# Kernel optimization log

Hardware: AMD Instinct MI355X
Metric: run time of the kernel (lower is better)

## Reference

```python
import jax, jax.numpy as jnp
import numpy as np

EMBED = 256      # hp.embed_size
ATT = 256        # hp.attention_size
KSZ = 5          # hp.kernel_size
L = 4            # hp.decoder_layers
N_MELS = 80
R = 4
KEY_PR = (4096 // 4) / 512.0   # hp.max_frames // hp.r / hp.max_timesteps = 2.0
QUERY_PR = 1.0
SQRT_HALF = float(np.sqrt(0.5))


def _pos_enc(T, C, pos_rate):
    # Faithful to source: angle_rates = pos*pos_rate/10000^(2*(k//2)/C); pe = pos*angle_rates
    pos = jnp.arange(T, dtype=jnp.float32)[:, None]            # [T,1]
    k = jnp.arange(C)[None, :]                                  # [1,C]
    power = jnp.power(jnp.float32(10000.0), 2.0 * (k // 2).astype(jnp.float32) / C)
    angle = pos * (pos * pos_rate / power)                      # [T,C]
    return jnp.where(k % 2 == 0, jnp.sin(angle), jnp.cos(angle))[None]  # [1,T,C]


def _conv_block(x, w, b, dilation):
    # causal dilated Conv1D + GLU + scaled residual. x:[B,T,C], w:[K,C,2C]
    pad = (KSZ - 1) * dilation
    y = jax.lax.conv_general_dilated(
        x, w, window_strides=(1,), padding=[(pad, 0)], rhs_dilation=(dilation,),
        dimension_numbers=('NWC', 'WIO', 'NWC')) + b
    a, g = jnp.split(y, 2, axis=-1)
    return (x + a * jax.nn.sigmoid(g)) * SQRT_HALF


def _attention(x, keys, values, w1, b1, w2, b2, w3, b3, wo, bo):
    Tq, Tk, C = x.shape[1], keys.shape[1], x.shape[-1]
    q = x + _pos_enc(Tq, C, QUERY_PR)
    k = keys + _pos_enc(Tk, C, KEY_PR)
    k_out = k @ w1 + b1           # fc1(keys)
    q_out = q @ w2 + b2           # fc2(query)
    v_out = values @ w3 + b3      # fc3(values)
    aw = jnp.einsum('bqd,bkd->bqk', q_out, k_out)
    # key_masks = ones_like(sum(keys_out,-1)) -> never zero, masking is a no-op (kept faithful)
    al = jax.nn.softmax(aw, axis=-1)  # dropout disabled (training=False)
    ctx = jnp.einsum('bqk,bkd->bqd', al, v_out) * jax.lax.rsqrt(jnp.float32(Tk))
    return ctx @ wo + bo


def setup_inputs() -> dict:
    key = jax.random.key(0)
    ks = jax.random.split(key, 16)
    s = jnp.float32(0.02)
    B, TQ, TK = 32, 1024, 512
    d = {}
    d['inputs'] = jax.random.normal(ks[0], (B, TQ, N_MELS * R), jnp.float32)
    d['keys'] = jax.random.normal(ks[1], (B, TK, EMBED), jnp.float32)
    d['values'] = jax.random.normal(ks[2], (B, TK, EMBED), jnp.float32)
    d['w_first'] = jax.random.normal(ks[3], (N_MELS * R, EMBED), jnp.float32) * s
    d['b_first'] = jnp.zeros((EMBED,), jnp.float32)
    d['fc_w'] = jax.random.normal(ks[4], (L - 1, EMBED, EMBED), jnp.float32) * s
    d['fc_b'] = jnp.zeros((L - 1, EMBED), jnp.float32)
    d['conv_w'] = jax.random.normal(ks[5], (L, KSZ, EMBED, 2 * EMBED), jnp.float32) * s
    d['conv_b'] = jnp.zeros((L, 2 * EMBED), jnp.float32)
    d['att_w1'] = jax.random.normal(ks[6], (L, EMBED, ATT), jnp.float32) * s
    d['att_b1'] = jnp.zeros((L, ATT), jnp.float32)
    d['att_w2'] = jax.random.normal(ks[7], (L, EMBED, ATT), jnp.float32) * s
    d['att_b2'] = jnp.zeros((L, ATT), jnp.float32)
    d['att_w3'] = jax.random.normal(ks[8], (L, EMBED, ATT), jnp.float32) * s
    d['att_b3'] = jnp.zeros((L, ATT), jnp.float32)
    d['att_wo'] = jax.random.normal(ks[9], (L, ATT, EMBED), jnp.float32) * s
    d['att_bo'] = jnp.zeros((L, EMBED), jnp.float32)
    d['w_done'] = jax.random.normal(ks[10], (EMBED, 2), jnp.float32) * s
    d['b_done'] = jnp.zeros((2,), jnp.float32)
    d['w_mel'] = jax.random.normal(ks[11], (EMBED, N_MELS * R), jnp.float32) * s
    d['b_mel'] = jnp.zeros((N_MELS * R,), jnp.float32)
    return d


def reference(inputs, keys, values, w_first, b_first, fc_w, fc_b, conv_w, conv_b,
              att_w1, att_b1, att_w2, att_b2, att_w3, att_b3, att_wo, att_bo,
              w_done, b_done, w_mel, b_mel):
    h = jax.nn.relu(inputs @ w_first + b_first)
    for i in range(L - 1):
        h = jax.nn.relu(h @ fc_w[i] + fc_b[i])
    for i in range(L):
        h = _conv_block(h, conv_w[i], conv_b[i], 2 ** i)
        att = _attention(h, keys, values,
                         att_w1[i], att_b1[i], att_w2[i], att_b2[i],
                         att_w3[i], att_b3[i], att_wo[i], att_bo[i])
        h = (att + h) * SQRT_HALF
    done_output = jax.nn.sigmoid(h @ w_done + b_done)
    mel_output = h @ w_mel + b_mel
    return (mel_output, done_output, h)
```

## Files before the change

### kernel.cpp

```cpp
#include <hip/hip_runtime.h>
#include <hip/hip_bf16.h>
#include <math.h>

#define SQH 0.70710678118654752440f

typedef __bf16 bf16x8 __attribute__((ext_vector_type(8)));
typedef float f32x4 __attribute__((ext_vector_type(4)));

__device__ __forceinline__ void glds16(const void* g, void* l) {
    __builtin_amdgcn_global_load_lds((const __attribute__((address_space(1))) void*)g,
                                     (__attribute__((address_space(3))) void*)l, 16, 0, 0);
}
__device__ __forceinline__ void wait_vm0_barrier() {
    asm volatile("s_waitcnt vmcnt(0)" ::: "memory");
    __builtin_amdgcn_s_barrier();
}

__device__ __forceinline__ int xcd_swz(int lin, int n) {
    if (n & 7) return lin;
    return (lin & 7) * (n >> 3) + (lin >> 3);
}

__global__ void pos_enc_kernel(float* __restrict__ pe, int T, float rate) {
    int idx = blockIdx.x * blockDim.x + threadIdx.x;
    if (idx >= T * 256) return;
    int t = idx >> 8;
    int k = idx & 255;
    float e = 2.0f * (float)(k >> 1) / 256.0f;
    float pw = powf(10000.0f, e);
    float ang = (float)t * ((float)t * rate / pw);
    pe[idx] = ((k & 1) == 0) ? sinf(ang) : cosf(ang);
}

__global__ void zero_init(float* z) { z[threadIdx.x] = 0.f; }

__global__ __launch_bounds__(256) void cvt_bf(const float* __restrict__ src,
                                              __bf16* __restrict__ dst, long n8) {
    long i = (long)blockIdx.x * 256 + threadIdx.x;
    if (i >= n8) return;
    const float* s = src + i * 8;
    float4 a = *(const float4*)s, b = *(const float4*)(s + 4);
    bf16x8 o;
    o[0] = (__bf16)a.x; o[1] = (__bf16)a.y; o[2] = (__bf16)a.z; o[3] = (__bf16)a.w;
    o[4] = (__bf16)b.x; o[5] = (__bf16)b.y; o[6] = (__bf16)b.z; o[7] = (__bf16)b.w;
    *(bf16x8*)(dst + i * 8) = o;
}

__global__ __launch_bounds__(256) void kpe_kernel(const float* __restrict__ keys,
                                                  const float* __restrict__ pek,
                                                  __bf16* __restrict__ dst) {
    long i = (long)blockIdx.x * 256 + threadIdx.x;
    long row = i >> 5; int c8 = (int)(i & 31) << 3;
    const float* kp = keys + row * 256 + c8;
    const float* pp = pek + (row & 511) * 256 + c8;
    float4 a = *(const float4*)kp, b = *(const float4*)(kp + 4);
    float4 p = *(const float4*)pp, q = *(const float4*)(pp + 4);
    bf16x8 o;
    o[0] = (__bf16)(a.x + p.x); o[1] = (__bf16)(a.y + p.y);
    o[2] = (__bf16)(a.z + p.z); o[3] = (__bf16)(a.w + p.w);
    o[4] = (__bf16)(b.x + q.x); o[5] = (__bf16)(b.y + q.y);
    o[6] = (__bf16)(b.z + q.z); o[7] = (__bf16)(b.w + q.w);
    *(bf16x8*)(dst + i * 8) = o;
}

__global__ __launch_bounds__(256) void transpose_k(const float* __restrict__ src,
                                                   __bf16* __restrict__ dst,
                                                   int R, int Cc, long sS, long sD) {
    __shared__ float tile[32][33];
    src += (long)blockIdx.z * sS;
    dst += (long)blockIdx.z * sD;
    int c0 = blockIdx.x * 32, r0 = blockIdx.y * 32;
    int tx = threadIdx.x & 31, ty = threadIdx.x >> 5;
#pragma unroll
    for (int p = 0; p < 4; ++p)
        tile[ty + 8 * p][tx] = src[(long)(r0 + ty + 8 * p) * Cc + c0 + tx];
    __syncthreads();
#pragma unroll
    for (int p = 0; p < 4; ++p)
        dst[(long)(c0 + ty + 8 * p) * R + r0 + tx] = (__bf16)tile[tx][ty + 8 * p];
}

template<int BIAS_MODE, int ACT, int OUT_MODE, int RES>
__global__ __launch_bounds__(256) void gemm_bf(
    const __bf16* __restrict__ A, const __bf16* __restrict__ Bt,
    const float* __restrict__ bias, const float* __restrict__ res,
    float* __restrict__ outF, __bf16* __restrict__ outB,
    int M, int N, int K, long sA, long sB, long sC)
{
    __shared__ __align__(16) __bf16 As[2][4096];
    __shared__ __align__(16) __bf16 Bs[2][4096];
    const int gx = gridDim.x, gy = gridDim.y;
    int lin = (blockIdx.z * gy + blockIdx.y) * gx + blockIdx.x;
    lin = xcd_swz(lin, gx * gy * gridDim.z);
    const int bx = lin % gx, by = (lin / gx) % gy, z = lin / (gx * gy);
    A += (long)z * sA;
    Bt += (long)z * sB;
    const int row0 = by << 7, col0 = bx << 7;
    const int tid = threadIdx.x, wid = tid >> 6, lane = tid & 63;
    const int lrow = lane & 15, lkp = lane >> 4;
    const int wm = (wid >> 1) << 6, wn = (wid & 1) << 6;
    const int srow = (wid << 5) + (lane >> 2);
    const int kq8 = (lane & 3) << 3;
    const __bf16* Ap0 = A + (long)(row0 + srow) * K + kq8;
    const __bf16* Ap1 = Ap0 + (long)16 * K;
    int c0i = col0 + srow, c1i = col0 + srow + 16;
    if (c0i > N - 1) c0i = N - 1;
    if (c1i > N - 1) c1i = N - 1;
    const __bf16* Bp0 = Bt + (long)c0i * K + kq8;
    const __bf16* Bp1 = Bt + (long)c1i * K + kq8;

    auto stage = [&](int b, int k0) {
        __bf16* A_ = As[b] + (wid << 10);
        __bf16* B_ = Bs[b] + (wid << 10);
        glds16(Ap0 + k0, A_);
        glds16(Ap1 + k0, A_ + 512);
        glds16(Bp0 + k0, B_);
        glds16(Bp1 + k0, B_ + 512);
    };

    f32x4 acc[4][4];
#pragma unroll
    for (int i = 0; i < 4; ++i)
#pragma unroll
        for (int j = 0; j < 4; ++j) acc[i][j] = (f32x4){0.f, 0.f, 0.f, 0.f};

    const int nk = K >> 5;
    stage(0, 0);
    wait_vm0_barrier();
    int cur = 0;
    for (int t = 0; t < nk; ++t) {
        if (t + 1 < nk) stage(cur ^ 1, (t + 1) << 5);
        bf16x8 af[4], bfr[4];
        const __bf16* Ar = As[cur] + (wm + lrow) * 32 + lkp * 8;
        const __bf16* Br = Bs[cur] + (wn + lrow) * 32 + lkp * 8;
#pragma unroll
        for (int i = 0; i < 4; ++i) af[i] = *(const bf16x8*)(Ar + i * 512);
#pragma unroll
        for (int j = 0; j < 4; ++j) bfr[j] = *(const bf16x8*)(Br + j * 512);
#pragma unroll
        for (int i = 0; i < 4; ++i)
#pragma unroll
            for (int j = 0; j < 4; ++j)
                acc[i][j] = __builtin_amdgcn_mfma_f32_16x16x32_bf16(af[i], bfr[j], acc[i][j], 0, 0, 0);
        wait_vm0_barrier();
        cur ^= 1;
    }

    float* oF = outF ? outF + (long)z * sC : nullptr;
    __bf16* oB = outB ? outB + (long)z * sC : nullptr;
    const float* resp = RES ? res + (long)z * sC : nullptr;
#pragma unroll
    for (int i = 0; i < 4; ++i) {
#pragma unroll
        for (int r = 0; r < 4; ++r) {
            const int gr = row0 + wm + i * 16 + lkp * 4 + r;
#pragma unroll
            for (int j = 0; j < 4; ++j) {
                const int gc = col0 + wn + j * 16 + lrow;
                if (gc >= N) continue;
                float v = acc[i][j][r];
                if (BIAS_MODE == 1) v += bias[gc];
                if (BIAS_MODE == 2) v += bias[gr];
                if (RES) v = (v + resp[(long)gr * N + gc]) * SQH;
                if (ACT == 1) v = fmaxf(v, 0.f);
                if (OUT_MODE == 0 || OUT_MODE == 2) oF[(long)gr * N + gc] = v;
                if (OUT_MODE == 1 || OUT_MODE == 2) oB[(long)gr * N + gc] = (__bf16)v;
            }
        }
    }
}

__global__ __launch_bounds__(256) void conv_glu(
    const __bf16* __restrict__ hbf, const float* __restrict__ hin,
    const __bf16* __restrict__ Wt, const float* __restrict__ bias,
    const float* __restrict__ peq,
    float* __restrict__ hc_f, __bf16* __restrict__ hc_b, __bf16* __restrict__ hq_b,
    int dil, const __bf16* __restrict__ zp)
{
    __shared__ __align__(16) __bf16 As[2][4096];
    __shared__ __align__(16) __bf16 Bas[2][2048];
    __shared__ __align__(16) __bf16 Bgs[2][2048];
    const int gx = gridDim.x;
    int lin = blockIdx.y * gx + blockIdx.x;
    lin = xcd_swz(lin, gx * gridDim.y);
    const int bx = lin % gx, by = lin / gx;
    const int row0 = by << 7, col0 = bx << 6;
    const int tid = threadIdx.x, wid = tid >> 6, lane = tid & 63;
    const int lrow = lane & 15, lkp = lane >> 4;
    const int wr = wid >> 1, wc = wid & 1;
    const int sA = (wid << 5) + (lane >> 2);
    const int kq8 = (lane & 3) << 3;
    const int grow = row0 + sA;
    const int t0 = (row0 & 1023) + sA;
    const int cB = col0 + (wid << 4) + (lane >> 2);
    const __bf16* Ba0 = Wt + (long)cB * 1280 + kq8;
    const __bf16* Bg0 = Wt + (long)(cB + 256) * 1280 + kq8;

    auto stage = [&](int b, int k0) {
        const int tap = k0 >> 8;
        const int off = (4 - tap) * dil;
        const int kc = (k0 & 255) + kq8;
        const __bf16* a0 = (t0 >= off) ? hbf + (long)(grow - off) * 256 + kc : zp;
        const __bf16* a1 = (t0 + 16 >= off) ? hbf + (long)(grow + 16 - off) * 256 + kc : zp;
        __bf16* A_ = As[b] + (wid << 10);
        glds16(a0, A_);
        glds16(a1, A_ + 512);
        glds16(Ba0 + k0, Bas[b] + (wid << 9));
        glds16(Bg0 + k0, Bgs[b] + (wid << 9));
    };

    f32x4 aca[4][2], acg[4][2];
#pragma unroll
    for (int i = 0; i < 4; ++i)
#pragma unroll
        for (int j = 0; j < 2; ++j) {
            aca[i][j] = (f32x4){0.f, 0.f, 0.f, 0.f};
            acg[i][j] = (f32x4){0.f, 0.f, 0.f, 0.f};
        }

    stage(0, 0);
    wait_vm0_barrier();
    int cur = 0;
    for (int t = 0; t < 40; ++t) {
        if (t + 1 < 40) stage(cur ^ 1, (t + 1) << 5);
        bf16x8 af[4], ba[2], bg[2];
        const __bf16* Ar = As[cur] + ((wr << 6) + lrow) * 32 + lkp * 8;
        const __bf16* Bar = Bas[cur] + ((wc << 5) + lrow) * 32 + lkp * 8;
        const __bf16* Bgr = Bgs[cur] + ((wc << 5) + lrow) * 32 + lkp * 8;
#pragma unroll
        for (int i = 0; i < 4; ++i) af[i] = *(const bf16x8*)(Ar + i * 512);
#pragma unroll
        for (int j = 0; j < 2; ++j) { ba[j] = *(const bf16x8*)(Bar + j * 512); bg[j] = *(const bf16x8*)(Bgr + j * 512); }
#pragma unroll
        for (int i = 0; i < 4; ++i)
#pragma unroll
            for (int j = 0; j < 2; ++j) {
                aca[i][j] = __builtin_amdgcn_mfma_f32_16x16x32_bf16(af[i], ba[j], aca[i][j], 0, 0, 0);
                acg[i][j] = __builtin_amdgcn_mfma_f32_16x16x32_bf16(af[i], bg[j], acg[i][j], 0, 0, 0);
            }
        wait_vm0_barrier();
        cur ^= 1;
    }
#pragma unroll
    for (int i = 0; i < 4; ++i) {
#pragma unroll
        for (int r = 0; r < 4; ++r) {
            const int gr = row0 + (wr << 6) + i * 16 + lkp * 4 + r;
            const long rb = (long)gr * 256;
            const long pb = (long)(gr & 1023) * 256;
#pragma unroll
            for (int j = 0; j < 2; ++j) {
                const int ca = col0 + (wc << 5) + j * 16 + lrow;
                float a = aca[i][j][r] + bias[ca];
                float g = acg[i][j][r] + bias[ca + 256];
                float v = (hin[rb + ca] + a / (1.f + expf(-g))) * SQH;
                hc_f[rb + ca] = v;
                hc_b[rb + ca] = (__bf16)v;
                hq_b[rb + ca] = (__bf16)(v + peq[pb + ca]);
            }
        }
    }
}

__global__ __launch_bounds__(512) void scores_sm(
    const __bf16* __restrict__ Q, const __bf16* __restrict__ Kb,
    __bf16* __restrict__ aw)
{
    __shared__ __align__(16) __bf16 As[2][128 * 32];
    __shared__ __align__(16) __bf16 Bs[2][512 * 32];
    __shared__ float redM[4][128];
    __shared__ float redS[4][128];
    int lin = xcd_swz(blockIdx.x, gridDim.x);
    const int rt = lin & 7, z = lin >> 3;
    const int row0 = rt << 7;
    const __bf16* Az = Q + (long)z * 1024 * 256;
    const __bf16* Bz = Kb + (long)z * 512 * 256;
    __bf16* awz = aw + (long)z * 1024 * 512;
    const int tid = threadIdx.x, wid = tid >> 6, lane = tid & 63;
    const int lrow = lane & 15, lkp = lane >> 4;
    const int wr = wid >> 2, wc = wid & 3;
    const int sr = lane >> 2;
    const int kq8 = (lane & 3) << 3;

    auto stage = [&](int b, int k0) {
        glds16(Az + (long)(row0 + (wid << 4) + sr) * 256 + k0 + kq8, As[b] + (wid << 9));
#pragma unroll
        for (int c = 0; c < 4; ++c) {
            const int R = ((c << 3) + wid) << 4;
            glds16(Bz + (long)(R + sr) * 256 + k0 + kq8, Bs[b] + (R << 5));
        }
    };

    f32x4 acc[4][8];
#pragma unroll
    for (int i = 0; i < 4; ++i)
#pragma unroll
        for (int j = 0; j < 8; ++j) acc[i][j] = (f32x4){0.f, 0.f, 0.f, 0.f};

    stage(0, 0);
    wait_vm0_barrier();
    int cur = 0;
    for (int t = 0; t < 8; ++t) {
        if (t + 1 < 8) stage(cur ^ 1, (t + 1) << 5);
        bf16x8 af[4], bfr[8];
        const __bf16* Ar = As[cur] + ((wr << 6) + lrow) * 32 + lkp * 8;
        const __bf16* Br = Bs[cur] + ((wc << 7) + lrow) * 32 + lkp * 8;
#pragma unroll
        for (int i = 0; i < 4; ++i) af[i] = *(const bf16x8*)(Ar + i * 512);
#pragma unroll
        for (int j = 0; j < 8; ++j) bfr[j] = *(const bf16x8*)(Br + j * 512);
#pragma unroll
        for (int i = 0; i < 4; ++i)
#pragma unroll
            for (int j = 0; j < 8; ++j)
                acc[i][j] = __builtin_amdgcn_mfma_f32_16x16x32_bf16(af[i], bfr[j], acc[i][j], 0, 0, 0);
        wait_vm0_barrier();
        cur ^= 1;
    }

    float mx[4][4];
#pragma unroll
    for (int i = 0; i < 4; ++i)
#pragma unroll
        for (int r = 0; r < 4; ++r) {
            float m = acc[i][0][r];
#pragma unroll
            for (int j = 1; j < 8; ++j) m = fmaxf(m, acc[i][j][r]);
#pragma unroll
            for (int s = 1; s < 16; s <<= 1) m = fmaxf(m, __shfl_xor(m, s));
            mx[i][r] = m;
        }
    if (lrow == 0) {
#pragma unroll
        for (int i = 0; i < 4; ++i)
#pragma unroll
            for (int r = 0; r < 4; ++r)
                redM[wc][(wr << 6) + i * 16 + (lkp << 2) + r] = mx[i][r];
    }
    __syncthreads();
    float sm[4][4];
#pragma unroll
    for (int i = 0; i < 4; ++i)
#pragma unroll
        for (int r = 0; r < 4; ++r) {
            const int row = (wr << 6) + i * 16 + (lkp << 2) + r;
            float m = fmaxf(fmaxf(redM[0][row], redM[1][row]), fmaxf(redM[2][row], redM[3][row]));
            float s = 0.f;
#pragma unroll
            for (int j = 0; j < 8; ++j) {
                float p = expf(acc[i][j][r] - m);
                acc[i][j][r] = p;
                s += p;
            }
#pragma unroll
            for (int sft = 1; sft < 16; sft <<= 1) s += __shfl_xor(s, sft);
            sm[i][r] = s;
        }
    if (lrow == 0) {
#pragma unroll
        for (int i = 0; i < 4; ++i)
#pragma unroll
            for (int r = 0; r < 4; ++r)
                redS[wc][(wr << 6) + i * 16 + (lkp << 2) + r] = sm[i][r];
    }
    __syncthreads();
#pragma unroll
    for (int i = 0; i < 4; ++i)
#pragma unroll
        for (int r = 0; r < 4; ++r) {
            const int row = (wr << 6) + i * 16 + (lkp << 2) + r;
            float S = redS[0][row] + redS[1][row] + redS[2][row] + redS[3][row];
            float sc = 0.04419417382415922f / S;
            __bf16* op = awz + (long)(row0 + row) * 512 + (wc << 7) + lrow;
#pragma unroll
            for (int j = 0; j < 8; ++j)
                op[j * 16] = (__bf16)(acc[i][j][r] * sc);
        }
}

__global__ __launch_bounds__(256) void done_kernel(const float* __restrict__ h,
                                                   const float* __restrict__ w,
                                                   const float* __restrict__ b,
                                                   float* __restrict__ out) {
    int row = blockIdx.x * 4 + (threadIdx.x >> 6);
    int lane = threadIdx.x & 63;
    float4 hv = *(const float4*)(h + (long)row * 256 + lane * 4);
    float4 w0 = *(const float4*)(w + lane * 8);
    float4 w1 = *(const float4*)(w + lane * 8 + 4);
    float d0 = hv.x * w0.x + hv.y * w0.z + hv.z * w1.x + hv.w * w1.z;
    float d1 = hv.x * w0.y + hv.y * w0.w + hv.z * w1.y + hv.w * w1.w;
#pragma unroll
    for (int s = 32; s; s >>= 1) { d0 += __shfl_xor(d0, s); d1 += __shfl_xor(d1, s); }
    if (lane == 0) {
        out[(long)row * 2 + 0] = 1.f / (1.f + expf(-(d0 + b[0])));
        out[(long)row * 2 + 1] = 1.f / (1.f + expf(-(d1 + b[1])));
    }
}

extern "C" void kernel_launch(void* const* d_in, const int* in_sizes, int n_in,
                              void* d_out, int out_size, void* d_ws, size_t ws_size,
                              hipStream_t stream) {
    const float* inputs  = (const float*)d_in[0];
    const float* keys    = (const float*)d_in[1];
    const float* values  = (const float*)d_in[2];
    const float* w_first = (const float*)d_in[3];
    const float* b_first = (const float*)d_in[4];
    const float* fc_w    = (const float*)d_in[5];
    const float* fc_b    = (const float*)d_in[6];
    const float* conv_w  = (const float*)d_in[7];
    const float* conv_b  = (const float*)d_in[8];
    const float* w1 = (const float*)d_in[9];  const float* b1 = (const float*)d_in[10];
    const float* w2 = (const float*)d_in[11]; const float* b2 = (const float*)d_in[12];
    const float* w3 = (const float*)d_in[13]; const float* b3 = (const float*)d_in[14];
    const float* wo = (const float*)d_in[15]; const float* bo = (const float*)d_in[16];
    const float* w_done = (const float*)d_in[17]; const float* b_done = (const float*)d_in[18];
    const float* w_mel  = (const float*)d_in[19]; const float* b_mel  = (const float*)d_in[20];
    float* out = (float*)d_out;
    float* ws  = (float*)d_ws;

    float* peq  = ws;
    float* pek  = peq + 262144;
    float* zp   = pek + 131072;
    float* h_f  = zp + 64;
    float* hc_f = h_f + 8388608;
    __bf16* h_b   = (__bf16*)(hc_f + 8388608);
    __bf16* hc_b  = h_b   + 8388608;
    __bf16* hq_b  = hc_b  + 8388608;
    __bf16* q_bf  = hq_b  + 8388608;
    __bf16* k_bf  = q_bf  + 8388608;
    __bf16* kpe_bf= k_bf  + 4194304;
    __bf16* val_bf= kpe_bf+ 4194304;
    __bf16* vT_bf = val_bf+ 4194304;
    __bf16* awb   = vT_bf + 4194304;
    __bf16* wfT   = awb   + 16777216;
    __bf16* fcT   = wfT   + 81920;
    __bf16* convT = fcT   + 196608;
    __bf16* w1T   = convT + 2621440;
    __bf16* w2T   = w1T   + 262144;
    __bf16* w3T   = w2T   + 262144;
    __bf16* woT   = w3T   + 262144;
    __bf16* wmT   = woT   + 262144;
    __bf16* in_bf = awb;
    __bf16* ctx_bf = q_bf;

    dim3 blk(256);

    pos_enc_kernel<<<1024, 256, 0, stream>>>(peq, 1024, 1.0f);
    pos_enc_kernel<<<512, 256, 0, stream>>>(pek, 512, 2.0f);
    zero_init<<<1, 64, 0, stream>>>(zp);

    cvt_bf<<<5120, 256, 0, stream>>>(inputs, in_bf, 1310720);
    cvt_bf<<<2048, 256, 0, stream>>>(values, val_bf, 524288);
    kpe_kernel<<<2048, 256, 0, stream>>>(keys, pek, kpe_bf);

    transpose_k<<<dim3(8, 10, 1), blk, 0, stream>>>(w_first, wfT, 320, 256, 0, 0);
    transpose_k<<<dim3(8, 8, 3), blk, 0, stream>>>(fc_w, fcT, 256, 256, 65536, 65536);
    transpose_k<<<dim3(16, 40, 4), blk, 0, stream>>>(conv_w, convT, 1280, 512, 655360, 655360);
    transpose_k<<<dim3(8, 8, 4), blk, 0, stream>>>(w1, w1T, 256, 256, 65536, 65536);
    transpose_k<<<dim3(8, 8, 4), blk, 0, stream>>>(w2, w2T, 256, 256, 65536, 65536);
    transpose_k<<<dim3(8, 8, 4), blk, 0, stream>>>(w3, w3T, 256, 256, 65536, 65536);
    transpose_k<<<dim3(8, 8, 4), blk, 0, stream>>>(wo, woT, 256, 256, 65536, 65536);
    transpose_k<<<dim3(10, 8, 1), blk, 0, stream>>>(w_mel, wmT, 256, 320, 0, 0);

    gemm_bf<1, 1, 1, 0><<<dim3(2, 256, 1), blk, 0, stream>>>(
        in_bf, wfT, b_first, nullptr, nullptr, h_b, 32768, 256, 320, 0, 0, 0);
    gemm_bf<1, 1, 1, 0><<<dim3(2, 256, 1), blk, 0, stream>>>(
        h_b, fcT + 0 * 65536, fc_b + 0 * 256, nullptr, nullptr, hq_b, 32768, 256, 256, 0, 0, 0);
    gemm_bf<1, 1, 1, 0><<<dim3(2, 256, 1), blk, 0, stream>>>(
        hq_b, fcT + 1 * 65536, fc_b + 1 * 256, nullptr, nullptr, hc_b, 32768, 256, 256, 0, 0, 0);
    gemm_bf<1, 1, 2, 0><<<dim3(2, 256, 1), blk, 0, stream>>>(
        hc_b, fcT + 2 * 65536, fc_b + 2 * 256, nullptr, h_f, h_b, 32768, 256, 256, 0, 0, 0);

    for (int l = 0; l < 4; ++l) {
        int dil = 1 << l;
        conv_glu<<<dim3(4, 256, 1), blk, 0, stream>>>(
            h_b, h_f, convT + (long)l * 655360, conv_b + l * 512, peq,
            hc_f, hc_b, hq_b, dil, (const __bf16*)zp);
        gemm_bf<1, 0, 1, 0><<<dim3(2, 256, 1), blk, 0, stream>>>(
            hq_b, w2T + (long)l * 65536, b2 + l * 256, nullptr, nullptr, q_bf, 32768, 256, 256, 0, 0, 0);
        gemm_bf<1, 0, 1, 0><<<dim3(2, 128, 1), blk, 0, stream>>>(
            kpe_bf, w1T + (long)l * 65536, b1 + l * 256, nullptr, nullptr, k_bf, 16384, 256, 256, 0, 0, 0);
        gemm_bf<2, 0, 1, 0><<<dim3(4, 2, 32), blk, 0, stream>>>(
            w3T + (long)l * 65536, val_bf, b3 + l * 256, nullptr, nullptr, vT_bf,
            256, 512, 256, 0, 512 * 256, 256 * 512);
        scores_sm<<<256, 512, 0, stream>>>(q_bf, k_bf, awb);
        gemm_bf<0, 0, 1, 0><<<dim3(2, 8, 32), blk, 0, stream>>>(
            awb, vT_bf, nullptr, nullptr, nullptr, ctx_bf,
            1024, 256, 512, 1024 * 512, 256 * 512, 1024 * 256);
        gemm_bf<1, 0, 2, 1><<<dim3(2, 256, 1), blk, 0, stream>>>(
            ctx_bf, woT + (long)l * 65536, bo + l * 256, hc_f, h_f, h_b, 32768, 256, 256, 0, 0, 0);
    }

    gemm_bf<1, 0, 0, 0><<<dim3(3, 256, 1), blk, 0, stream>>>(
        h_b, wmT, b_mel, nullptr, out, nullptr, 32768, 320, 256, 0, 0, 0);
    done_kernel<<<8192, 256, 0, stream>>>(h_f, w_done, b_done, out + 10485760);
    hipMemcpyAsync(out + 10551296, h_f, (size_t)8388608 * 4, hipMemcpyDeviceToDevice, stream);
}
```

Before: 1.236 ms.

## Overlap prefetch with compute, reorder LDS staging, batch key projections

The GEMM, conv_glu and scores kernels now wait only for the current stage's loads (vmcnt(4)/vmcnt(5)) before the barrier. The next stage's global-to-LDS loads can then overlap the MFMA work instead of being drained at the end of each iteration. Lane-to-row mapping for staging and the LDS read addressing change to a k-major layout, which may reduce bank conflicts. All four layers' key projections (fc1 of keys) are computed in one batched launch up front, and the unused hc_b bf16 store is dropped. The partial vmcnt wait depends on how many loads are in flight and on in-order completion, which risks correctness if the counts are wrong.

```diff
diff --git a/kernel.cpp b/kernel.cpp
--- a/kernel.cpp
+++ b/kernel.cpp
@@ -10,10 +10,6 @@
 __device__ __forceinline__ void glds16(const void* g, void* l) {
     __builtin_amdgcn_global_load_lds((const __attribute__((address_space(1))) void*)g,
                                      (__attribute__((address_space(3))) void*)l, 16, 0, 0);
-}
-__device__ __forceinline__ void wait_vm0_barrier() {
-    asm volatile("s_waitcnt vmcnt(0)" ::: "memory");
-    __builtin_amdgcn_s_barrier();
 }
 
 __device__ __forceinline__ int xcd_swz(int lin, int n) {
@@ -85,7 +81,7 @@
     const __bf16* __restrict__ A, const __bf16* __restrict__ Bt,
     const float* __restrict__ bias, const float* __restrict__ res,
     float* __restrict__ outF, __bf16* __restrict__ outB,
-    int M, int N, int K, long sA, long sB, long sC)
+    int M, int N, int K, long sA, long sB, long sC, long sBias, int zmB)
 {
     __shared__ __align__(16) __bf16 As[2][4096];
     __shared__ __align__(16) __bf16 Bs[2][4096];
@@ -94,13 +90,14 @@
     lin = xcd_swz(lin, gx * gy * gridDim.z);
     const int bx = lin % gx, by = (lin / gx) % gy, z = lin / (gx * gy);
     A += (long)z * sA;
-    Bt += (long)z * sB;
+    Bt += (long)(z % zmB) * sB;
+    bias = bias ? bias + (long)z * sBias : bias;
     const int row0 = by << 7, col0 = bx << 7;
     const int tid = threadIdx.x, wid = tid >> 6, lane = tid & 63;
     const int lrow = lane & 15, lkp = lane >> 4;
     const int wm = (wid >> 1) << 6, wn = (wid & 1) << 6;
-    const int srow = (wid << 5) + (lane >> 2);
-    const int kq8 = (lane & 3) << 3;
+    const int srow = (wid << 5) + (lane & 15);
+    const int kq8 = (lane >> 4) << 3;
     const __bf16* Ap0 = A + (long)(row0 + srow) * K + kq8;
     const __bf16* Ap1 = Ap0 + (long)16 * K;
     int c0i = col0 + srow, c1i = col0 + srow + 16;
@@ -125,24 +122,30 @@
         for (int j = 0; j < 4; ++j) acc[i][j] = (f32x4){0.f, 0.f, 0.f, 0.f};
 
     const int nk = K >> 5;
+    const int ab = (wm >> 4), bb = (wn >> 4);
     stage(0, 0);
-    wait_vm0_barrier();
     int cur = 0;
     for (int t = 0; t < nk; ++t) {
-        if (t + 1 < nk) stage(cur ^ 1, (t + 1) << 5);
+        if (t + 1 < nk) {
+            stage(cur ^ 1, (t + 1) << 5);
+            asm volatile("s_waitcnt vmcnt(4)" ::: "memory");
+        } else {
+            asm volatile("s_waitcnt vmcnt(0)" ::: "memory");
+        }
+        __builtin_amdgcn_s_barrier();
         bf16x8 af[4], bfr[4];
-        const __bf16* Ar = As[cur] + (wm + lrow) * 32 + lkp * 8;
-        const __bf16* Br = Bs[cur] + (wn + lrow) * 32 + lkp * 8;
-#pragma unroll
-        for (int i = 0; i < 4; ++i) af[i] = *(const bf16x8*)(Ar + i * 512);
-#pragma unroll
-        for (int j = 0; j < 4; ++j) bfr[j] = *(const bf16x8*)(Br + j * 512);
+#pragma unroll
+        for (int i = 0; i < 4; ++i)
+            af[i] = *(const bf16x8*)(As[cur] + (ab + i) * 512 + lkp * 128 + lrow * 8);
+#pragma unroll
+        for (int j = 0; j < 4; ++j)
+            bfr[j] = *(const bf16x8*)(Bs[cur] + (bb + j) * 512 + lkp * 128 + lrow * 8);
 #pragma unroll
         for (int i = 0; i < 4; ++i)
 #pragma unroll
             for (int j = 0; j < 4; ++j)
                 acc[i][j] = __builtin_amdgcn_mfma_f32_16x16x32_bf16(af[i], bfr[j], acc[i][j], 0, 0, 0);
-        wait_vm0_barrier();
+        __builtin_amdgcn_s_barrier();
         cur ^= 1;
     }
 
@@ -174,7 +177,7 @@
     const __bf16* __restrict__ hbf, const float* __restrict__ hin,
     const __bf16* __restrict__ Wt, const float* __restrict__ bias,
     const float* __restrict__ peq,
-    float* __restrict__ hc_f, __bf16* __restrict__ hc_b, __bf16* __restrict__ hq_b,
+    float* __restrict__ hc_f, __bf16* __restrict__ hq_b,
     int dil, const __bf16* __restrict__ zp)
 {
     __shared__ __align__(16) __bf16 As[2][4096];
@@ -188,11 +191,11 @@
     const int tid = threadIdx.x, wid = tid >> 6, lane = tid & 63;
     const int lrow = lane & 15, lkp = lane >> 4;
     const int wr = wid >> 1, wc = wid & 1;
-    const int sA = (wid << 5) + (lane >> 2);
-    const int kq8 = (lane & 3) << 3;
-    const int grow = row0 + sA;
-    const int t0 = (row0 & 1023) + sA;
-    const int cB = col0 + (wid << 4) + (lane >> 2);
+    const int srowA = (wid << 5) + (lane & 15);
+    const int kq8 = (lane >> 4) << 3;
+    const int grow = row0 + srowA;
+    const int t0 = (row0 & 1023) + srowA;
+    const int cB = col0 + (wid << 4) + (lane & 15);
     const __bf16* Ba0 = Wt + (long)cB * 1280 + kq8;
     const __bf16* Bg0 = Wt + (long)(cB + 256) * 1280 + kq8;
 
@@ -219,18 +222,24 @@
         }
 
     stage(0, 0);
-    wait_vm0_barrier();
     int cur = 0;
     for (int t = 0; t < 40; ++t) {
-        if (t + 1 < 40) stage(cur ^ 1, (t + 1) << 5);
+        if (t + 1 < 40) {
+            stage(cur ^ 1, (t + 1) << 5);
+            asm volatile("s_waitcnt vmcnt(4)" ::: "memory");
+        } else {
+            asm volatile("s_waitcnt vmcnt(0)" ::: "memory");
+        }
+        __builtin_amdgcn_s_barrier();
         bf16x8 af[4], ba[2], bg[2];
-        const __bf16* Ar = As[cur] + ((wr << 6) + lrow) * 32 + lkp * 8;
-        const __bf16* Bar = Bas[cur] + ((wc << 5) + lrow) * 32 + lkp * 8;
-        const __bf16* Bgr = Bgs[cur] + ((wc << 5) + lrow) * 32 + lkp * 8;
-#pragma unroll
-        for (int i = 0; i < 4; ++i) af[i] = *(const bf16x8*)(Ar + i * 512);
-#pragma unroll
-        for (int j = 0; j < 2; ++j) { ba[j] = *(const bf16x8*)(Bar + j * 512); bg[j] = *(const bf16x8*)(Bgr + j * 512); }
+#pragma unroll
+        for (int i = 0; i < 4; ++i)
+            af[i] = *(const bf16x8*)(As[cur] + ((wr << 2) + i) * 512 + lkp * 128 + lrow * 8);
+#pragma unroll
+        for (int j = 0; j < 2; ++j) {
+            ba[j] = *(const bf16x8*)(Bas[cur] + ((wc << 1) + j) * 512 + lkp * 128 + lrow * 8);
+            bg[j] = *(const bf16x8*)(Bgs[cur] + ((wc << 1) + j) * 512 + lkp * 128 + lrow * 8);
+        }
 #pragma unroll
         for (int i = 0; i < 4; ++i)
 #pragma unroll
@@ -238,7 +247,7 @@
                 aca[i][j] = __builtin_amdgcn_mfma_f32_16x16x32_bf16(af[i], ba[j], aca[i][j], 0, 0, 0);
                 acg[i][j] = __builtin_amdgcn_mfma_f32_16x16x32_bf16(af[i], bg[j], acg[i][j], 0, 0, 0);
             }
-        wait_vm0_barrier();
+        __builtin_amdgcn_s_barrier();
         cur ^= 1;
     }
 #pragma unroll
@@ -255,7 +264,6 @@
                 float g = acg[i][j][r] + bias[ca + 256];
                 float v = (hin[rb + ca] + a / (1.f + expf(-g))) * SQH;
                 hc_f[rb + ca] = v;
-                hc_b[rb + ca] = (__bf16)v;
                 hq_b[rb + ca] = (__bf16)(v + peq[pb + ca]);
             }
         }
@@ -279,8 +287,8 @@
     const int tid = threadIdx.x, wid = tid >> 6, lane = tid & 63;
     const int lrow = lane & 15, lkp = lane >> 4;
     const int wr = wid >> 2, wc = wid & 3;
-    const int sr = lane >> 2;
-    const int kq8 = (lane & 3) << 3;
+    const int sr = lane & 15;
+    const int kq8 = (lane >> 4) << 3;
 
     auto stage = [&](int b, int k0) {
         glds16(Az + (long)(row0 + (wid << 4) + sr) * 256 + k0 + kq8, As[b] + (wid << 9));
@@ -298,23 +306,28 @@
         for (int j = 0; j < 8; ++j) acc[i][j] = (f32x4){0.f, 0.f, 0.f, 0.f};
 
     stage(0, 0);
-    wait_vm0_barrier();
     int cur = 0;
     for (int t = 0; t < 8; ++t) {
-        if (t + 1 < 8) stage(cur ^ 1, (t + 1) << 5);
+        if (t + 1 < 8) {
+            stage(cur ^ 1, (t + 1) << 5);
+            asm volatile("s_waitcnt vmcnt(5)" ::: "memory");
+        } else {
+            asm volatile("s_waitcnt vmcnt(0)" ::: "memory");
+        }
+        __builtin_amdgcn_s_barrier();
         bf16x8 af[4], bfr[8];
-        const __bf16* Ar = As[cur] + ((wr << 6) + lrow) * 32 + lkp * 8;
-        const __bf16* Br = Bs[cur] + ((wc << 7) + lrow) * 32 + lkp * 8;
-#pragma unroll
-        for (int i = 0; i < 4; ++i) af[i] = *(const bf16x8*)(Ar + i * 512);
-#pragma unroll
-        for (int j = 0; j < 8; ++j) bfr[j] = *(const bf16x8*)(Br + j * 512);
+#pragma unroll
+        for (int i = 0; i < 4; ++i)
+            af[i] = *(const bf16x8*)(As[cur] + ((wr << 2) + i) * 512 + lkp * 128 + lrow * 8);
+#pragma unroll
+        for (int j = 0; j < 8; ++j)
+            bfr[j] = *(const bf16x8*)(Bs[cur] + ((wc << 3) + j) * 512 + lkp * 128 + lrow * 8);
 #pragma unroll
         for (int i = 0; i < 4; ++i)
 #pragma unroll
             for (int j = 0; j < 8; ++j)
                 acc[i][j] = __builtin_amdgcn_mfma_f32_16x16x32_bf16(af[i], bfr[j], acc[i][j], 0, 0, 0);
-        wait_vm0_barrier();
+        __builtin_amdgcn_s_barrier();
         cur ^= 1;
     }
 
@@ -417,6 +430,7 @@
     const float* w_mel  = (const float*)d_in[19]; const float* b_mel  = (const float*)d_in[20];
     float* out = (float*)d_out;
     float* ws  = (float*)d_ws;
+    const int BIG = 1 << 30;
 
     float* peq  = ws;
     float* pek  = peq + 262144;
@@ -424,14 +438,13 @@
     float* h_f  = zp + 64;
     float* hc_f = h_f + 8388608;
     __bf16* h_b   = (__bf16*)(hc_f + 8388608);
-    __bf16* hc_b  = h_b   + 8388608;
-    __bf16* hq_b  = hc_b  + 8388608;
+    __bf16* hq_b  = h_b   + 8388608;
     __bf16* q_bf  = hq_b  + 8388608;
-    __bf16* k_bf  = q_bf  + 8388608;
-    __bf16* kpe_bf= k_bf  + 4194304;
+    __bf16* kpe_bf= q_bf  + 8388608;
     __bf16* val_bf= kpe_bf+ 4194304;
     __bf16* vT_bf = val_bf+ 4194304;
-    __bf16* awb   = vT_bf + 4194304;
+    __bf16* k_all = vT_bf + 4194304;
+    __bf16* awb   = k_all + 16777216;
     __bf16* wfT   = awb   + 16777216;
     __bf16* fcT   = wfT   + 81920;
     __bf16* convT = fcT   + 196608;
@@ -462,37 +475,41 @@
     transpose_k<<<dim3(8, 8, 4), blk, 0, stream>>>(wo, woT, 256, 256, 65536, 65536);
     transpose_k<<<dim3(10, 8, 1), blk, 0, stream>>>(w_mel, wmT, 256, 320, 0, 0);
 
+    gemm_bf<1, 0, 1, 0><<<dim3(2, 128, 4), blk, 0, stream>>>(
+        kpe_bf, w1T, b1, nullptr, nullptr, k_all,
+        16384, 256, 256, 0, 65536, 4194304, 256, BIG);
+
     gemm_bf<1, 1, 1, 0><<<dim3(2, 256, 1), blk, 0, stream>>>(
-        in_bf, wfT, b_first, nullptr, nullptr, h_b, 32768, 256, 320, 0, 0, 0);
+        in_bf, wfT, b_first, nullptr, nullptr, h_b, 32768, 256, 320, 0, 0, 0, 0, BIG);
     gemm_bf<1, 1, 1, 0><<<dim3(2, 256, 1), blk, 0, stream>>>(
-        h_b, fcT + 0 * 65536, fc_b + 0 * 256, nullptr, nullptr, hq_b, 32768, 256, 256, 0, 0, 0);
+        h_b, fcT + 0 * 65536, fc_b + 0 * 256, nullptr, nullptr, hq_b, 32768, 256, 256, 0, 0, 0, 0, BIG);
     gemm_bf<1, 1, 1, 0><<<dim3(2, 256, 1), blk, 0, stream>>>(
-        hq_b, fcT + 1 * 65536, fc_b + 1 * 256, nullptr, nullptr, hc_b, 32768, 256, 256, 0, 0, 0);
+        hq_b, fcT + 1 * 65536, fc_b + 1 * 256, nullptr, nullptr, q_bf, 32768, 256, 256, 0, 0, 0, 0, BIG);
     gemm_bf<1, 1, 2, 0><<<dim3(2, 256, 1), blk, 0, stream>>>(
-        hc_b, fcT + 2 * 65536, fc_b + 2 * 256, nullptr, h_f, h_b, 32768, 256, 256, 0, 0, 0);
+        q_bf, fcT + 2 * 65536, fc_b + 2 * 256, nullptr, h_f, h_b, 32768, 256, 256, 0, 0, 0, 0, BIG);
 
     for (int l = 0; l < 4; ++l) {
         int dil = 1 << l;
         conv_glu<<<dim3(4, 256, 1), blk, 0, stream>>>(
             h_b, h_f, convT + (long)l * 655360, conv_b + l * 512, peq,
-            hc_f, hc_b, hq_b, dil, (const __bf16*)zp);
+            hc_f, hq_b, dil, (const __bf16*)zp);
         gemm_bf<1, 0, 1, 0><<<dim3(2, 256, 1), blk, 0, stream>>>(
-            hq_b, w2T + (long)l * 65536, b2 + l * 256, nullptr, nullptr, q_bf, 32768, 256, 256, 0, 0, 0);
-        gemm_bf<1, 0, 1, 0><<<dim3(2, 128, 1), blk, 0, stream>>>(
-            kpe_bf, w1T + (long)l * 65536, b1 + l * 256, nullptr, nullptr, k_bf, 16384, 256, 256, 0, 0, 0);
+            hq_b, w2T + (long)l * 65536, b2 + l * 256, nullptr, nullptr, q_bf,
+            32768, 256, 256, 0, 0, 0, 0, BIG);
         gemm_bf<2, 0, 1, 0><<<dim3(4, 2, 32), blk, 0, stream>>>(
             w3T + (long)l * 65536, val_bf, b3 + l * 256, nullptr, nullptr, vT_bf,
-            256, 512, 256, 0, 512 * 256, 256 * 512);
-        scores_sm<<<256, 512, 0, stream>>>(q_bf, k_bf, awb);
+            256, 512, 256, 0, 131072, 131072, 0, BIG);
+        scores_sm<<<256, 512, 0, stream>>>(q_bf, k_all + (long)l * 4194304, awb);
         gemm_bf<0, 0, 1, 0><<<dim3(2, 8, 32), blk, 0, stream>>>(
             awb, vT_bf, nullptr, nullptr, nullptr, ctx_bf,
-            1024, 256, 512, 1024 * 512, 256 * 512, 1024 * 256);
+            1024, 256, 512, 1024 * 512, 131072, 262144, 0, BIG);
         gemm_bf<1, 0, 2, 1><<<dim3(2, 256, 1), blk, 0, stream>>>(
-            ctx_bf, woT + (long)l * 65536, bo + l * 256, hc_f, h_f, h_b, 32768, 256, 256, 0, 0, 0);
+            ctx_bf, woT + (long)l * 65536, bo + l * 256, hc_f, h_f, h_b,
+            32768, 256, 256, 0, 0, 0, 0, BIG);
     }
 
     gemm_bf<1, 0, 0, 0><<<dim3(3, 256, 1), blk, 0, stream>>>(
-        h_b, wmT, b_mel, nullptr, out, nullptr, 32768, 320, 256, 0, 0, 0);
+        h_b, wmT, b_mel, nullptr, out, nullptr, 32768, 320, 256, 0, 0, 0, 0, BIG);
     done_kernel<<<8192, 256, 0, stream>>>(h_f, w_done, b_done, out + 10485760);
     hipMemcpyAsync(out + 10551296, h_f, (size_t)8388608 * 4, hipMemcpyDeviceToDevice, stream);
 }
```

New measurement: 1.417 ms. 14.6% more time.
